# Optimization experiments

Measured on AMD Instinct MI355X. Metric: run time of the kernel, lower is better.

The kernel has to match this reference:

```python
import jax, jax.numpy as jnp
import numpy as np

B, T, D = 4, 4096, 2048
R = 512  # config.r; greedy always finds R pairs since R <= ceil((T-1)/3)
EPS = 1e-12  # F.normalize eps


def setup_inputs() -> dict:
    key = jax.random.key(0)
    x = jax.random.normal(key, (B, T, D), dtype=jnp.float32)
    return {"x": x}


def _select_pairs(adj):
    """Greedy non-overlapping adjacent pair selection (== find_merge_pairs).

    adj: (T-1,) similarity of (i, i+1). Returns sel: (T-1,) bool marking the
    first index i of each selected pair, exactly R pairs.
    """
    order = jnp.argsort(-adj)  # descending, stable (matches stable python sort)

    def step(carry, i):
        used, sel, count = carry
        ok = (~used[i]) & (~used[i + 1]) & (count < R)
        used = used.at[i].set(used[i] | ok)
        used = used.at[i + 1].set(used[i + 1] | ok)
        sel = sel.at[i].set(ok)
        return (used, sel, count + ok.astype(jnp.int32)), None

    init = (jnp.zeros(T, dtype=bool), jnp.zeros(T - 1, dtype=bool), jnp.int32(0))
    (_, sel, _), _ = jax.lax.scan(step, init, order)
    return sel


def reference(x) -> jnp.ndarray:
    # --- similarity (torch.no_grad in original -> stop_gradient) ---
    xs = jax.lax.stop_gradient(x)
    norm = jnp.maximum(jnp.linalg.norm(xs, axis=-1, keepdims=True), EPS)
    xn = xs / norm
    sim = jnp.einsum('btd,bsd->bts', xn, xn)  # (B,T,T) full matrix, as original
    idx = jnp.arange(T - 1)
    adj = sim[0, idx, idx + 1]                 # adjacent similarities of batch 0

    # --- find_merge_pairs ---
    sel = _select_pairs(adj)                   # (T-1,) bool, first index of pair
    sel_pad = jnp.concatenate([sel, jnp.zeros(1, dtype=bool)])      # (T,)
    rem = jnp.concatenate([jnp.zeros(1, dtype=bool), sel])          # (T,) removed j's
    keep = ~rem

    # --- merge_tokens (mode='mean'): x[i] <- (x[i]+x[i+1])/2, drop x[j] ---
    x_next = jnp.concatenate([x[:, 1:], x[:, -1:]], axis=1)
    merged_vals = 0.5 * (x + x_next)
    x_mod = jnp.where(sel_pad[None, :, None], merged_vals, x)
    kept_idx = jnp.nonzero(keep, size=T - R, fill_value=0)[0]       # static size
    x_merged = x_mod[:, kept_idx]             # (B, T-R, D)

    # --- base_layer = identity ---
    out = x_merged

    # --- unmerge_tokens: duplicate merged token back into position j ---
    src = jnp.cumsum(keep.astype(jnp.int32)) - 1   # original pos -> merged index
    return out[:, src]                              # (B, T, D)
```

## Files before the change

### kernel.cpp

```cpp
#include <hip/hip_runtime.h>

#define B_ 4
#define T_ 4096
#define D_ 2048
#define R_ 512
#define NPAIR (T_ - 1)
#define EPS_ 1e-12f

__global__ __launch_bounds__(256) void adj_fused_k(const float* __restrict__ x,
                                                   float* __restrict__ adj) {
    const int i = blockIdx.x;
    const float4* r0 = (const float4*)(x + (size_t)i * D_);
    const float4* r1 = (const float4*)(x + (size_t)(i + 1) * D_);
    float4 a0 = r0[threadIdx.x], a1 = r0[threadIdx.x + 256];
    float4 b0 = r1[threadIdx.x], b1 = r1[threadIdx.x + 256];

    float sa = a0.x * a0.x + a0.y * a0.y + a0.z * a0.z + a0.w * a0.w +
               a1.x * a1.x + a1.y * a1.y + a1.z * a1.z + a1.w * a1.w;
    float sb = b0.x * b0.x + b0.y * b0.y + b0.z * b0.z + b0.w * b0.w +
               b1.x * b1.x + b1.y * b1.y + b1.z * b1.z + b1.w * b1.w;
    #pragma unroll
    for (int off = 1; off < 64; off <<= 1) {
        sa += __shfl_xor(sa, off, 64);
        sb += __shfl_xor(sb, off, 64);
    }
    __shared__ float wsa[4], wsb[4], wss[4];
    const int w = threadIdx.x >> 6;
    if ((threadIdx.x & 63) == 0) { wsa[w] = sa; wsb[w] = sb; }
    __syncthreads();
    const float ni = fmaxf(sqrtf(wsa[0] + wsa[1] + wsa[2] + wsa[3]), EPS_);
    const float nj = fmaxf(sqrtf(wsb[0] + wsb[1] + wsb[2] + wsb[3]), EPS_);

    float s = (a0.x / ni) * (b0.x / nj) + (a0.y / ni) * (b0.y / nj) +
              (a0.z / ni) * (b0.z / nj) + (a0.w / ni) * (b0.w / nj) +
              (a1.x / ni) * (b1.x / nj) + (a1.y / ni) * (b1.y / nj) +
              (a1.z / ni) * (b1.z / nj) + (a1.w / ni) * (b1.w / nj);
    #pragma unroll
    for (int off = 1; off < 64; off <<= 1) s += __shfl_xor(s, off, 64);
    if ((threadIdx.x & 63) == 0) wss[w] = s;
    __syncthreads();
    if (threadIdx.x == 0) adj[i] = wss[0] + wss[1] + wss[2] + wss[3];
}

__global__ __launch_bounds__(256) void select_k(const float* __restrict__ adj,
                                                int* __restrict__ m_out) {
    __shared__ unsigned long long ka[T_];
    __shared__ unsigned char state[T_];
    __shared__ unsigned char dec[T_];
    __shared__ int hist[256];
    __shared__ int sflag;
    __shared__ int sneed;
    __shared__ unsigned long long thrsh;
    const int tid = threadIdx.x;

    for (int i = tid; i < T_; i += 256) {
        if (i < NPAIR) {
            unsigned u = __float_as_uint(adj[i]);
            u ^= (u & 0x80000000u) ? 0xFFFFFFFFu : 0x80000000u;
            ka[i] = ((unsigned long long)u << 32) | (unsigned)(NPAIR - 1 - i);
            state[i] = 0;
        } else {
            ka[i] = 0ull;
            state[i] = 2;
        }
    }
    __syncthreads();

    for (;;) {
        if (tid == 0) sflag = 0;
        for (int i = tid; i < NPAIR; i += 256) {
            bool acc = false;
            if (state[i] == 0) {
                unsigned long long k = ka[i];
                bool okl = (i == 0)         || state[i - 1] != 0 || k > ka[i - 1];
                bool okr = (i == NPAIR - 1) || state[i + 1] != 0 || k > ka[i + 1];
                acc = okl && okr;
            }
            dec[i] = acc ? 1 : 0;
        }
        __syncthreads();
        bool anyLive = false;
        for (int i = tid; i < NPAIR; i += 256) {
            unsigned char st = state[i];
            if (st == 0) {
                if (dec[i]) st = 1;
                else if ((i > 0 && dec[i - 1]) || (i < NPAIR - 1 && dec[i + 1])) st = 2;
                state[i] = st;
                anyLive |= (st == 0);
            }
        }
        if (anyLive) sflag = 1;
        __syncthreads();
        if (sflag == 0) break;
    }

    if (tid == 0) { thrsh = 0ull; sneed = R_; }
    for (int byte = 7; byte >= 0; --byte) {
        hist[tid] = 0;
        __syncthreads();
        const int shift = byte * 8;
        for (int i = tid; i < NPAIR; i += 256) {
            if (state[i] == 1) {
                unsigned long long k = ka[i];
                bool match = (byte == 7) || ((k >> (shift + 8)) == (thrsh >> (shift + 8)));
                if (match) atomicAdd(&hist[(int)((k >> shift) & 0xFF)], 1);
            }
        }
        __syncthreads();
        if (tid < 64) {
            const int l = tid;
            int c0 = hist[4 * l], c1 = hist[4 * l + 1], c2 = hist[4 * l + 2], c3 = hist[4 * l + 3];
            int g = c0 + c1 + c2 + c3;
            int G = g;
            #pragma unroll
            for (int off = 1; off < 64; off <<= 1) {
                int o = __shfl_down(G, off, 64);
                G += (l + off < 64) ? o : 0;
            }
            const int aboveGroup = G - g;
            const int need = sneed;
            int ca3 = aboveGroup;
            int ca2 = ca3 + c3;
            int ca1 = ca2 + c2;
            int ca0 = ca1 + c1;
            int selv = -1, selca = 0;
            if      (ca3 < need && need <= ca3 + c3) { selv = 4 * l + 3; selca = ca3; }
            else if (ca2 < need && need <= ca2 + c2) { selv = 4 * l + 2; selca = ca2; }
            else if (ca1 < need && need <= ca1 + c1) { selv = 4 * l + 1; selca = ca1; }
            else if (ca0 < need && need <= ca0 + c0) { selv = 4 * l + 0; selca = ca0; }
            if (selv >= 0) {
                thrsh |= ((unsigned long long)(unsigned)selv) << shift;
                sneed = need - selca;
            }
        }
        __syncthreads();
    }

    const unsigned long long thr = thrsh;
    for (int i = tid; i < T_; i += 256) {
        int mv = 0;
        if (i < NPAIR && state[i] == 1 && ka[i] >= thr) mv = 1;
        else if (i > 0 && state[i - 1] == 1 && ka[i - 1] >= thr) mv = 2;
        m_out[i] = mv;
    }
}

__global__ __launch_bounds__(256) void apply_merge_k(const float* __restrict__ x,
                                                     const int* __restrict__ m,
                                                     float* __restrict__ out) {
    const int D4 = D_ / 4;
    const int total = B_ * T_ * D4;
    const float4* xv = (const float4*)x;
    float4* ov = (float4*)out;
    for (int idx = blockIdx.x * 256 + threadIdx.x; idx < total;
         idx += gridDim.x * 256) {
        int row = idx >> 9;
        int t = row & (T_ - 1);
        int mm = m[t];
        float4 v = xv[idx];
        if (mm) {
            int off = (mm == 1) ? D4 : -D4;
            float4 w = xv[idx + off];
            v.x = 0.5f * (v.x + w.x);
            v.y = 0.5f * (v.y + w.y);
            v.z = 0.5f * (v.z + w.z);
            v.w = 0.5f * (v.w + w.w);
        }
        ov[idx] = v;
    }
}

extern "C" void kernel_launch(void* const* d_in, const int* in_sizes, int n_in,
                              void* d_out, int out_size, void* d_ws, size_t ws_size,
                              hipStream_t stream) {
    const float* x = (const float*)d_in[0];
    float* out = (float*)d_out;
    float* adj = (float*)d_ws;
    int* m = (int*)(adj + T_);

    adj_fused_k<<<NPAIR, 256, 0, stream>>>(x, adj);
    select_k<<<1, 256, 0, stream>>>(adj, m);
    apply_merge_k<<<8192, 256, 0, stream>>>(x, m, out);
}
```

Before: 284.0 us.

## Run greedy pair-selection rounds as single-wavefront bitmask propagation

The iterative local-maximum selection loop, which used two block-wide barriers per round over byte state arrays, is replaced by one 64-lane wavefront. Each lane holds 64-bit masks that precompute left/right dominance, and each round is resolved with shifts, shuffles and a ballot, with no block barriers. Accepted pairs are stored as a 64-word bitmask used by the threshold radix select and the final mark pass. The aim is to cut the serial latency of the single-block select kernel. The trade-off is that only 64 of the 256 threads do work during this phase.

```diff
diff --git a/kernel.cpp b/kernel.cpp
--- a/kernel.cpp
+++ b/kernel.cpp
@@ -6,6 +6,7 @@
 #define R_ 512
 #define NPAIR (T_ - 1)
 #define EPS_ 1e-12f
+typedef unsigned long long ull;
 
 __global__ __launch_bounds__(256) void adj_fused_k(const float* __restrict__ x,
                                                    float* __restrict__ adj) {
@@ -44,65 +45,67 @@
 
 __global__ __launch_bounds__(256) void select_k(const float* __restrict__ adj,
                                                 int* __restrict__ m_out) {
-    __shared__ unsigned long long ka[T_];
-    __shared__ unsigned char state[T_];
-    __shared__ unsigned char dec[T_];
+    __shared__ ull ka[T_];
+    __shared__ ull accM[64];
     __shared__ int hist[256];
-    __shared__ int sflag;
     __shared__ int sneed;
-    __shared__ unsigned long long thrsh;
+    __shared__ ull thrsh;
     const int tid = threadIdx.x;
 
     for (int i = tid; i < T_; i += 256) {
         if (i < NPAIR) {
             unsigned u = __float_as_uint(adj[i]);
             u ^= (u & 0x80000000u) ? 0xFFFFFFFFu : 0x80000000u;
-            ka[i] = ((unsigned long long)u << 32) | (unsigned)(NPAIR - 1 - i);
-            state[i] = 0;
+            ka[i] = ((ull)u << 32) | (unsigned)(NPAIR - 1 - i);
         } else {
             ka[i] = 0ull;
-            state[i] = 2;
         }
+    }
+    if (tid == 0) { thrsh = 0ull; sneed = R_; }
+    __syncthreads();
+
+    if (tid < 64) {
+        const int lane = tid;
+        ull GL = 0, GR = 0;
+        for (int g = 0; g < 64; ++g) {
+            const int i = g * 64 + lane;
+            const ull k = ka[i];
+            bool gl = (i == 0) || (k > ka[i - 1]);
+            bool gr = (i >= NPAIR - 1) || (k > ka[i + 1]);
+            ull bgl = __ballot(gl);
+            ull bgr = __ballot(gr);
+            if (lane == g) { GL = bgl; GR = bgr; }
+        }
+        ull live = ~0ull;
+        if (lane == 63) live &= ~(1ull << 63);
+        ull acc = 0;
+        for (;;) {
+            ull upl = __shfl_up(live, 1, 64);
+            ull dnl = __shfl_down(live, 1, 64);
+            ull liveL = (live << 1) | ((lane == 0) ? 0ull : (upl >> 63));
+            ull liveR = (live >> 1) | ((lane == 63) ? 0ull : (dnl << 63));
+            ull a = live & (~liveL | GL) & (~liveR | GR);
+            ull upa = __shfl_up(a, 1, 64);
+            ull dna = __shfl_down(a, 1, 64);
+            ull aL = (a << 1) | ((lane == 0) ? 0ull : (upa >> 63));
+            ull aR = (a >> 1) | ((lane == 63) ? 0ull : (dna << 63));
+            acc |= a;
+            live &= ~(a | aL | aR);
+            if (__ballot(live != 0ull) == 0ull) break;
+        }
+        accM[lane] = acc;
     }
     __syncthreads();
 
-    for (;;) {
-        if (tid == 0) sflag = 0;
-        for (int i = tid; i < NPAIR; i += 256) {
-            bool acc = false;
-            if (state[i] == 0) {
-                unsigned long long k = ka[i];
-                bool okl = (i == 0)         || state[i - 1] != 0 || k > ka[i - 1];
-                bool okr = (i == NPAIR - 1) || state[i + 1] != 0 || k > ka[i + 1];
-                acc = okl && okr;
-            }
-            dec[i] = acc ? 1 : 0;
-        }
-        __syncthreads();
-        bool anyLive = false;
-        for (int i = tid; i < NPAIR; i += 256) {
-            unsigned char st = state[i];
-            if (st == 0) {
-                if (dec[i]) st = 1;
-                else if ((i > 0 && dec[i - 1]) || (i < NPAIR - 1 && dec[i + 1])) st = 2;
-                state[i] = st;
-                anyLive |= (st == 0);
-            }
-        }
-        if (anyLive) sflag = 1;
-        __syncthreads();
-        if (sflag == 0) break;
-    }
-
-    if (tid == 0) { thrsh = 0ull; sneed = R_; }
     for (int byte = 7; byte >= 0; --byte) {
+        const ull tcur = thrsh;
         hist[tid] = 0;
         __syncthreads();
         const int shift = byte * 8;
         for (int i = tid; i < NPAIR; i += 256) {
-            if (state[i] == 1) {
-                unsigned long long k = ka[i];
-                bool match = (byte == 7) || ((k >> (shift + 8)) == (thrsh >> (shift + 8)));
+            if ((accM[i >> 6] >> (i & 63)) & 1ull) {
+                const ull k = ka[i];
+                bool match = (byte == 7) || ((k >> (shift + 8)) == (tcur >> (shift + 8)));
                 if (match) atomicAdd(&hist[(int)((k >> shift) & 0xFF)], 1);
             }
         }
@@ -129,18 +132,20 @@
             else if (ca1 < need && need <= ca1 + c1) { selv = 4 * l + 1; selca = ca1; }
             else if (ca0 < need && need <= ca0 + c0) { selv = 4 * l + 0; selca = ca0; }
             if (selv >= 0) {
-                thrsh |= ((unsigned long long)(unsigned)selv) << shift;
+                thrsh |= ((ull)(unsigned)selv) << shift;
                 sneed = need - selca;
             }
         }
         __syncthreads();
     }
 
-    const unsigned long long thr = thrsh;
+    const ull thr = thrsh;
     for (int i = tid; i < T_; i += 256) {
         int mv = 0;
-        if (i < NPAIR && state[i] == 1 && ka[i] >= thr) mv = 1;
-        else if (i > 0 && state[i - 1] == 1 && ka[i - 1] >= thr) mv = 2;
+        bool self = (i < NPAIR) && ((accM[i >> 6] >> (i & 63)) & 1ull) && ka[i] >= thr;
+        bool left = (i > 0) && ((accM[(i - 1) >> 6] >> ((i - 1) & 63)) & 1ull) && ka[i - 1] >= thr;
+        if (self) mv = 1;
+        else if (left) mv = 2;
         m_out[i] = mv;
     }
 }
```

Result: faster. 269.1 us (-5.3%).
